# Kernel tuning notes

Hardware: AMD Instinct MI355X
Metric: run time of the kernel (lower is better)

The kernel has to match this reference:

```python
import jax, jax.numpy as jnp
import numpy as np

B, S, H = 512, 50, 20
N_NODE, N_CAT = 100000, 1298
MEM, CLUS = 20, 10
STEP, KBLOCKS = 1, 2
MIX = 0.52  # a = 0.52*attn_last + 0.48*ht


def setup_inputs() -> dict:
    key = jax.random.key(0)
    ks = iter(jax.random.split(key, 48))
    stdv = 1.0 / np.sqrt(H)
    def u(shape):
        return jax.random.uniform(next(ks), shape, jnp.float32, -stdv, stdv)
    inp = {}
    inp['inputs'] = jax.random.randint(next(ks), (B, S), 0, N_NODE, dtype=jnp.int32)
    inp['category'] = jax.random.randint(next(ks), (B, S), 0, N_CAT, dtype=jnp.int32)
    inp['A'] = jax.random.uniform(next(ks), (B, S, 2 * S), jnp.float32)
    inp['mask'] = jnp.ones((B, S), jnp.int32)
    # embeddings
    inp['emb'] = u((N_NODE, H)); inp['emb1'] = u((N_CAT, H))
    # GNN params
    inp['w_ih'] = u((3 * H, 2 * H)); inp['w_hh'] = u((3 * H, H))
    inp['b_ih'] = u((3 * H,)); inp['b_hh'] = u((3 * H,))
    inp['b_iah'] = u((H,)); inp['b_oah'] = u((H,))
    inp['w_ein'] = u((H, H)); inp['b_ein'] = u((H,))
    inp['w_eout'] = u((H, H)); inp['b_eout'] = u((H,))
    # two single-head MHAs
    for p in ('mha', 'mha1'):
        inp[p + '_in_w'] = u((3 * H, H)); inp[p + '_in_b'] = u((3 * H,))
        inp[p + '_out_w'] = u((H, H)); inp[p + '_out_b'] = u((H,))
    # residual blocks
    for p in ('rn', 'rn1'):
        inp[p + '_w1'] = u((H, H)); inp[p + '_b1'] = u((H,))
        inp[p + '_w2'] = u((H, H)); inp[p + '_b2'] = u((H,))
    # memory readout
    inp['mem_M'] = u((CLUS, MEM)); inp['mem_Wa'] = u((2 * H, MEM)); inp['mem_fc'] = u((MEM, MEM))
    # heads
    inp['wc'] = u((H, 3 * H)); inp['bc'] = u((H,))
    inp['wp'] = u((H, 3 * H)); inp['bp'] = u((H,))
    return inp


def _mha(x, w_in, b_in, w_out, b_out):
    # Faithful to torch nn.MultiheadAttention (seq-first, 1 head):
    # x is [B,S,H] but torch treats dim0 as sequence -> attention mixes along axis 0.
    E = x.shape[-1]
    q, k, v = jnp.split(x @ w_in.T + b_in, 3, axis=-1)
    q = q * (1.0 / jnp.sqrt(jnp.float32(E)))
    scores = jnp.einsum('lne,mne->nlm', q, k)        # [S_axis1, L, L]
    attn = jax.nn.softmax(scores, axis=-1)
    out = jnp.einsum('nlm,mne->lne', attn, v)
    return out @ w_out.T + b_out


def _residual(x, w1, b1, w2, b2):
    # eval mode: dropout = identity
    return x + jax.nn.relu(x @ w1.T + b1) @ w2.T + b2


def _gnn_cell(A, h, w_ein, b_ein, w_eout, b_eout, b_iah, b_oah, w_ih, b_ih, w_hh, b_hh):
    s = h.shape[1]
    inp_in = jnp.einsum('bij,bjh->bih', A[:, :, :s], h @ w_ein.T + b_ein) + b_iah
    inp_out = jnp.einsum('bij,bjh->bih', A[:, :, s:2 * s], h @ w_eout.T + b_eout) + b_oah
    gi = jnp.concatenate([inp_in, inp_out], -1) @ w_ih.T + b_ih
    gh = h @ w_hh.T + b_hh
    i_r, i_i, i_n = jnp.split(gi, 3, -1)
    h_r, h_i, h_n = jnp.split(gh, 3, -1)
    r = jax.nn.sigmoid(i_r + h_r)
    z = jax.nn.sigmoid(i_i + h_i)
    n = jnp.tanh(i_n + r * h_n)
    return n + z * (h - n)


def reference(inputs, category, A, mask, emb, emb1, w_ih, w_hh, b_ih, b_hh, b_iah, b_oah,
              w_ein, b_ein, w_eout, b_eout,
              mha_in_w, mha_in_b, mha_out_w, mha_out_b,
              mha1_in_w, mha1_in_b, mha1_out_w, mha1_out_b,
              rn_w1, rn_b1, rn_w2, rn_b2, rn1_w1, rn1_b1, rn1_w2, rn1_b2,
              mem_M, mem_Wa, mem_fc, wc, bc, wp, bp):
    item_h = emb[inputs]          # [B,S,H]
    cat_h = emb1[category]        # [B,S,H]
    for _ in range(STEP):
        item_h = _gnn_cell(A, item_h, w_ein, b_ein, w_eout, b_eout,
                           b_iah, b_oah, w_ih, b_ih, w_hh, b_hh)
    bidx = jnp.arange(mask.shape[0])
    last = jnp.sum(mask, 1) - 1
    ht_item = item_h[bidx, last]
    ht_cat = cat_h[bidx, last]
    x = item_h
    for _ in range(KBLOCKS):
        x = _residual(_mha(x, mha_in_w, mha_in_b, mha_out_w, mha_out_b), rn_w1, rn_b1, rn_w2, rn_b2)
    a_item = MIX * x[bidx, last] + (1 - MIX) * ht_item
    y = cat_h
    for _ in range(KBLOCKS):
        y = _residual(_mha(y, mha1_in_w, mha1_in_b, mha1_out_w, mha1_out_b), rn1_w1, rn1_b1, rn1_w2, rn1_b2)
    a_cat = MIX * y[bidx, last] + (1 - MIX) * ht_cat
    a = jnp.concatenate([a_item, a_cat], -1)                # [B, 2H]
    att = jax.nn.softmax((a @ mem_Wa) @ mem_M.T, axis=-1)   # [B, CLUS]
    reps = jnp.tanh((att @ mem_M) @ mem_fc)                 # [B, MEM]
    car = jnp.concatenate([a, reps], -1)                    # [B, 3H]
    final = jax.nn.sigmoid(car @ wc.T + bc) * (car @ wp.T + bp)
    scores = final @ emb[1:].T                              # [B, N_NODE-1]
    return scores
```

## Files before the change

### kernel.cpp

```cpp
#include <hip/hip_runtime.h>
#include <hip/hip_bf16.h>

#define BB 512
#define SS 50
#define HH 20
#define NN 100000
#define NMC 8
#define MCH 64
#define NRC 4
#define MT 16
#define PBSTRIDE ((size_t)BB*24)

__device__ __forceinline__ float frcp(float x){
#if __has_builtin(__builtin_amdgcn_rcpf)
  return __builtin_amdgcn_rcpf(x);
#else
  return 1.f/x;
#endif
}
__device__ __forceinline__ float fsig(float x){ return frcp(1.f + __expf(-x)); }
__device__ __forceinline__ float ftanh(float x){ return 1.f - 2.f*frcp(1.f + __expf(2.f*x)); }

__global__ __launch_bounds__(256)
void k_gnnqkv(const int* __restrict__ inputs, const int* __restrict__ category,
              const float* __restrict__ A, const int* __restrict__ mask,
              const float* __restrict__ emb, const float* __restrict__ emb1,
              const float* __restrict__ w_ih, const float* __restrict__ w_hh,
              const float* __restrict__ b_ih, const float* __restrict__ b_hh,
              const float* __restrict__ b_iah, const float* __restrict__ b_oah,
              const float* __restrict__ w_ein, const float* __restrict__ b_ein,
              const float* __restrict__ w_eout, const float* __restrict__ b_eout,
              const float* __restrict__ inw0, const float* __restrict__ inb0,
              const float* __restrict__ inw1, const float* __restrict__ inb1,
              float* __restrict__ q_t, float* __restrict__ k_t, float* __restrict__ v_t,
              int* __restrict__ last, float* __restrict__ ht_item, float* __restrict__ ht_cat)
{
    __shared__ float sA[SS*2*SS];
    __shared__ float sit[SS*HH], sct[SS*HH], shin[SS*HH], shout[SS*HH];
    __shared__ float sinp[SS*HH], soutp[SS*HH];
    __shared__ float swein[HH*HH], sweout[HH*HH];
    __shared__ float swih[60*40], swhh[60*HH];
    __shared__ float sw0[60*HH], sw1w[60*HH];
    __shared__ float sbein[HH], sbeout[HH], sbih[60], sbhh[60], sbiah[HH], sboah[HH], sb0[60], sb1b[60];
    __shared__ int slast;
    const int b = blockIdx.x, t = threadIdx.x;

    for (int i=t;i<SS*2*SS;i+=256) sA[i] = A[(size_t)b*SS*2*SS + i];
    for (int i=t;i<HH*HH;i+=256) { swein[i]=w_ein[i]; sweout[i]=w_eout[i]; }
    for (int i=t;i<60*40;i+=256) swih[i]=w_ih[i];
    for (int i=t;i<60*HH;i+=256) { swhh[i]=w_hh[i]; sw0[i]=inw0[i]; sw1w[i]=inw1[i]; }
    if (t<60){ sbih[t]=b_ih[t]; sbhh[t]=b_hh[t]; sb0[t]=inb0[t]; sb1b[t]=inb1[t]; }
    if (t<HH){ sbein[t]=b_ein[t]; sbeout[t]=b_eout[t]; sbiah[t]=b_iah[t]; sboah[t]=b_oah[t]; }
    for (int i=t;i<SS*HH;i+=256){
        int r=i/HH, e=i%HH;
        sit[i]=emb [(size_t)inputs  [b*SS+r]*HH+e];
        sct[i]=emb1[(size_t)category[b*SS+r]*HH+e];
    }
    if (t==0){ int s=0; for (int j=0;j<SS;j++) s+=mask[b*SS+j]; slast=s-1; }
    __syncthreads();

    for (int i=t;i<SS*HH;i+=256){
        int r=i/HH, c=i%HH;
        float si=sbein[c], so=sbeout[c];
        #pragma unroll
        for (int e=0;e<HH;e++){ float hv=sit[r*HH+e]; si+=swein[c*HH+e]*hv; so+=sweout[c*HH+e]*hv; }
        shin[i]=si; shout[i]=so;
    }
    __syncthreads();
    for (int i=t;i<SS*HH;i+=256){
        int r=i/HH, e=i%HH;
        float ai=sbiah[e], ao=sboah[e];
        #pragma unroll 5
        for (int j=0;j<SS;j++){
            ai+=sA[r*2*SS+j]   *shin [j*HH+e];
            ao+=sA[r*2*SS+SS+j]*shout[j*HH+e];
        }
        sinp[i]=ai; soutp[i]=ao;
    }
    __syncthreads();
    float nh[4];
    #pragma unroll
    for (int ii=0;ii<4;ii++){
        int i=t+ii*256;
        if (i<SS*HH){
            int r=i/HH, e=i%HH;
            float gir=sbih[e], gii=sbih[20+e], gin=sbih[40+e];
            #pragma unroll
            for (int k=0;k<HH;k++){
                float vi=sinp[r*HH+k], vo=soutp[r*HH+k];
                gir+=swih[e*40+k]*vi      + swih[e*40+HH+k]*vo;
                gii+=swih[(20+e)*40+k]*vi + swih[(20+e)*40+HH+k]*vo;
                gin+=swih[(40+e)*40+k]*vi + swih[(40+e)*40+HH+k]*vo;
            }
            float ghr=sbhh[e], ghi=sbhh[20+e], ghn=sbhh[40+e];
            #pragma unroll
            for (int k=0;k<HH;k++){
                float hv=sit[r*HH+k];
                ghr+=swhh[e*HH+k]*hv; ghi+=swhh[(20+e)*HH+k]*hv; ghn+=swhh[(40+e)*HH+k]*hv;
            }
            float rr=fsig(gir+ghr), zz=fsig(gii+ghi);
            float nn2=ftanh(gin+rr*ghn);
            nh[ii]=nn2+zz*(sit[i]-nn2);
        }
    }
    __syncthreads();
    #pragma unroll
    for (int ii=0;ii<4;ii++){ int i=t+ii*256; if (i<SS*HH) sit[i]=nh[ii]; }
    __syncthreads();

    if (t<HH)                    ht_item[b*HH+t]      = sit[slast*HH+t];
    else if (t>=32 && t<32+HH)   ht_cat [b*HH+(t-32)] = sct[slast*HH+(t-32)];
    else if (t==63)              last[b]=slast;

    const float SCALE = 0.22360679774997896f;
    for (int oi=t; oi<2*SS*60; oi+=256){
        int p=oi/(SS*60); int rem=oi%(SS*60); int r=rem/60; int c=rem%60;
        const float* src = p? sct  : sit;
        const float* w   = p? sw1w : sw0;
        const float* bb_ = p? sb1b : sb0;
        float acc=bb_[c];
        #pragma unroll
        for (int e=0;e<HH;e++) acc += w[c*HH+e]*src[r*HH+e];
        int which=c/HH, cc=c%HH;
        size_t off=((size_t)(p*SS+r)*BB + b)*HH + cc;
        if (which==0)      q_t[off]=acc*SCALE;
        else if (which==1) k_t[off]=acc;
        else               v_t[off]=acc;
    }
}

__global__ __launch_bounds__(256)
void k_flags(const int* __restrict__ last, int* __restrict__ needed)
{
    __shared__ int nf[SS];
    int t=threadIdx.x;
    if (t<SS) nf[t]=0;
    __syncthreads();
    for (int b=t;b<BB;b+=256){ int l=last[b]; atomicOr(&nf[l],1); }
    __syncthreads();
    if (t<SS) needed[t]=nf[t];
}

__global__ __launch_bounds__(128)
void k_attn(const float* __restrict__ q_t, const float* __restrict__ k_t,
            const float* __restrict__ v_t, const int* __restrict__ needed,
            float* __restrict__ pbuf)
{
    const int s=blockIdx.x, p=blockIdx.y, z=blockIdx.z;
    if (!needed[s]) return;
    const int mc=z>>2, rc=z&3, t=threadIdx.x;
    __shared__ float sk[MCH*HH], sv[MCH*HH];
    const size_t base=(size_t)(p*SS+s)*BB;
    {
        const float4* kb=(const float4*)(k_t+(base+(size_t)mc*MCH)*HH);
        const float4* vb=(const float4*)(v_t+(base+(size_t)mc*MCH)*HH);
        float4* sk4=(float4*)sk; float4* sv4=(float4*)sv;
        for (int i=t;i<MCH*HH/4;i+=128){ sk4[i]=kb[i]; sv4[i]=vb[i]; }
    }
    __syncthreads();
    const int row = rc*128 + t;
    float4 q[5];
    {
        const float4* qp=(const float4*)(q_t+(base+row)*HH);
        #pragma unroll
        for (int i=0;i<5;i++) q[i]=qp[i];
    }
    float4 o[5];
    #pragma unroll
    for (int i=0;i<5;i++) o[i]=make_float4(0.f,0.f,0.f,0.f);
    float mx=-1e30f, sm=0.f;

    for (int mt0=0; mt0<MCH; mt0+=MT){
        float sc[MT]; float tm=-1e30f;
        #pragma unroll
        for (int j=0;j<MT;j++){
            const float4* kr=(const float4*)(sk+(mt0+j)*HH);
            float a0=0.f;
            #pragma unroll
            for (int i=0;i<5;i++){
                float4 kv=kr[i];
                a0+=q[i].x*kv.x+q[i].y*kv.y+q[i].z*kv.z+q[i].w*kv.w;
            }
            sc[j]=a0; tm=fmaxf(tm,a0);
        }
        float nm=fmaxf(mx,tm);
        float c=__expf(mx-nm);
        sm*=c;
        #pragma unroll
        for (int i=0;i<5;i++){ o[i].x*=c; o[i].y*=c; o[i].z*=c; o[i].w*=c; }
        mx=nm;
        #pragma unroll
        for (int j=0;j<MT;j++){
            float pe=__expf(sc[j]-nm);
            sm+=pe;
            const float4* vr=(const float4*)(sv+(mt0+j)*HH);
            #pragma unroll
            for (int i=0;i<5;i++){
                float4 vv=vr[i];
                o[i].x+=pe*vv.x; o[i].y+=pe*vv.y; o[i].z+=pe*vv.z; o[i].w+=pe*vv.w;
            }
        }
    }
    float* pb = pbuf + (((size_t)(p*SS+s)*NMC+mc)*BB + row)*24;
    float4* w0=(float4*)pb;
    w0[0]=make_float4(mx,sm,o[0].x,o[0].y);
    w0[1]=make_float4(o[0].z,o[0].w,o[1].x,o[1].y);
    w0[2]=make_float4(o[1].z,o[1].w,o[2].x,o[2].y);
    w0[3]=make_float4(o[2].z,o[2].w,o[3].x,o[3].y);
    w0[4]=make_float4(o[3].z,o[3].w,o[4].x,o[4].y);
    w0[5]=make_float4(o[4].z,o[4].w,0.f,0.f);
}

__device__ __forceinline__ void merge_res(const float* __restrict__ pbase,
    const float* __restrict__ sow, const float* __restrict__ sob,
    const float* __restrict__ sw1, const float* __restrict__ sb1,
    const float* __restrict__ sw2, const float* __restrict__ sb2,
    float* __restrict__ xo)
{
    float mx=-1e30f;
    #pragma unroll
    for (int mc2=0;mc2<NMC;mc2++) mx=fmaxf(mx, pbase[mc2*PBSTRIDE]);
    float sum=0.f, o[HH];
    #pragma unroll
    for (int e=0;e<HH;e++) o[e]=0.f;
    #pragma unroll
    for (int mc2=0;mc2<NMC;mc2++){
        const float4* pc=(const float4*)(pbase+mc2*PBSTRIDE);
        float4 a=pc[0], b4=pc[1], c4=pc[2], d4=pc[3], e4=pc[4], f4=pc[5];
        float cc=__expf(a.x-mx);
        sum+=a.y*cc;
        o[0]+=a.z*cc;  o[1]+=a.w*cc;
        o[2]+=b4.x*cc; o[3]+=b4.y*cc; o[4]+=b4.z*cc; o[5]+=b4.w*cc;
        o[6]+=c4.x*cc; o[7]+=c4.y*cc; o[8]+=c4.z*cc; o[9]+=c4.w*cc;
        o[10]+=d4.x*cc; o[11]+=d4.y*cc; o[12]+=d4.z*cc; o[13]+=d4.w*cc;
        o[14]+=e4.x*cc; o[15]+=e4.y*cc; o[16]+=e4.z*cc; o[17]+=e4.w*cc;
        o[18]+=f4.x*cc; o[19]+=f4.y*cc;
    }
    float inv=frcp(sum);
    float ao[HH];
    #pragma unroll
    for (int e=0;e<HH;e++) ao[e]=o[e]*inv;
    float mo[HH];
    #pragma unroll
    for (int e=0;e<HH;e++){
        float acc=sob[e];
        #pragma unroll
        for (int f=0;f<HH;f++) acc+=sow[e*HH+f]*ao[f];
        mo[e]=acc;
    }
    float u[HH];
    #pragma unroll
    for (int g=0;g<HH;g++){
        float acc=sb1[g];
        #pragma unroll
        for (int f=0;f<HH;f++) acc+=sw1[g*HH+f]*mo[f];
        u[g]=fmaxf(acc,0.f);
    }
    #pragma unroll
    for (int e=0;e<HH;e++){
        float acc=mo[e]+sb2[e];
        #pragma unroll
        for (int g=0;g<HH;g++) acc+=sw2[e*HH+g]*u[g];
        xo[e]=acc;
    }
}

__global__ __launch_bounds__(256)
void k_finqkv(const float* __restrict__ pbuf, const int* __restrict__ needed,
    const float* __restrict__ ow0, const float* __restrict__ ob0,
    const float* __restrict__ w10, const float* __restrict__ b10,
    const float* __restrict__ w20, const float* __restrict__ b20,
    const float* __restrict__ iw0, const float* __restrict__ ib0,
    const float* __restrict__ ow1, const float* __restrict__ ob1,
    const float* __restrict__ w11, const float* __restrict__ b11,
    const float* __restrict__ w21, const float* __restrict__ b21,
    const float* __restrict__ iw1, const float* __restrict__ ib1,
    float* __restrict__ q_t, float* __restrict__ k_t, float* __restrict__ v_t)
{
    const int s=blockIdx.x>>1;
    if (!needed[s]) return;
    __shared__ float sow[400], sw1[400], sw2[400], siw[1200];
    __shared__ float sob[20], sb1[20], sb2[20], sib[60];
    const int p=blockIdx.y, t=threadIdx.x;
    const int b=(blockIdx.x&1)*256+t;
    const float* OW=p?ow1:ow0; const float* OB=p?ob1:ob0;
    const float* W1=p?w11:w10; const float* B1=p?b11:b10;
    const float* W2=p?w21:w20; const float* B2=p?b21:b20;
    const float* IW=p?iw1:iw0; const float* IB=p?ib1:ib0;
    for (int i=t;i<400;i+=256){ sow[i]=OW[i]; sw1[i]=W1[i]; sw2[i]=W2[i]; }
    for (int i=t;i<1200;i+=256) siw[i]=IW[i];
    if (t<20){ sob[t]=OB[t]; sb1[t]=B1[t]; sb2[t]=B2[t]; }
    if (t<60) sib[t]=IB[t];
    __syncthreads();
    const float* pbase = pbuf + (((size_t)(p*SS+s)*NMC)*BB + b)*24;
    float xo[HH];
    merge_res(pbase, sow,sob,sw1,sb1,sw2,sb2, xo);
    const float SCALE = 0.22360679774997896f;
    size_t off0=((size_t)(p*SS+s)*BB + b)*HH;
    #pragma unroll
    for (int c=0;c<HH;c++){
        float aq=sib[c], ak=sib[20+c], av=sib[40+c];
        #pragma unroll
        for (int e=0;e<HH;e++){ float xv=xo[e]; aq+=siw[c*HH+e]*xv; ak+=siw[(20+c)*HH+e]*xv; av+=siw[(40+c)*HH+e]*xv; }
        q_t[off0+c]=aq*SCALE; k_t[off0+c]=ak; v_t[off0+c]=av;
    }
}

__global__ __launch_bounds__(256)
void k_fin(const float* __restrict__ pbuf, const int* __restrict__ needed,
    const int* __restrict__ last,
    const float* __restrict__ ht_item, const float* __restrict__ ht_cat,
    const float* __restrict__ ow0, const float* __restrict__ ob0,
    const float* __restrict__ w10, const float* __restrict__ b10,
    const float* __restrict__ w20, const float* __restrict__ b20,
    const float* __restrict__ ow1, const float* __restrict__ ob1,
    const float* __restrict__ w11, const float* __restrict__ b11,
    const float* __restrict__ w21, const float* __restrict__ b21,
    float* __restrict__ a_out)
{
    const int s=blockIdx.x>>1;
    if (!needed[s]) return;
    __shared__ float sow[400], sw1[400], sw2[400];
    __shared__ float sob[20], sb1[20], sb2[20];
    const int p=blockIdx.y, t=threadIdx.x;
    const int b=(blockIdx.x&1)*256+t;
    const float* OW=p?ow1:ow0; const float* OB=p?ob1:ob0;
    const float* W1=p?w11:w10; const float* B1=p?b11:b10;
    const float* W2=p?w21:w20; const float* B2=p?b21:b20;
    for (int i=t;i<400;i+=256){ sow[i]=OW[i]; sw1[i]=W1[i]; sw2[i]=W2[i]; }
    if (t<20){ sob[t]=OB[t]; sb1[t]=B1[t]; sb2[t]=B2[t]; }
    __syncthreads();
    if (last[b] != s) return;
    const float* pbase = pbuf + (((size_t)(p*SS+s)*NMC)*BB + b)*24;
    float xo[HH];
    merge_res(pbase, sow,sob,sw1,sb1,sw2,sb2, xo);
    const float* ht = p? ht_cat : ht_item;
    #pragma unroll
    for (int e=0;e<HH;e++)
        a_out[(size_t)b*40 + p*HH + e] = 0.52f*xo[e] + 0.48f*ht[b*HH+e];
}

__global__ __launch_bounds__(64)
void k_head(const float* __restrict__ a_in,
            const float* __restrict__ mem_M, const float* __restrict__ mem_Wa,
            const float* __restrict__ mem_fc,
            const float* __restrict__ wc, const float* __restrict__ bc,
            const float* __restrict__ wp, const float* __restrict__ bp,
            float* __restrict__ final_)
{
    int b=blockIdx.x*64+threadIdx.x;
    if (b>=BB) return;
    float a[40];
    const float4* a4=(const float4*)(a_in+(size_t)b*40);
    #pragma unroll
    for (int i=0;i<10;i++){ float4 v=a4[i]; a[4*i]=v.x; a[4*i+1]=v.y; a[4*i+2]=v.z; a[4*i+3]=v.w; }
    float t20[20];
    #pragma unroll
    for (int j=0;j<20;j++){
        float acc=0.f;
        #pragma unroll
        for (int k=0;k<40;k++) acc+=a[k]*mem_Wa[k*20+j];
        t20[j]=acc;
    }
    float lg[10]; float mxv=-1e30f;
    #pragma unroll
    for (int c=0;c<10;c++){
        float acc=0.f;
        #pragma unroll
        for (int j=0;j<20;j++) acc+=t20[j]*mem_M[c*20+j];
        lg[c]=acc; mxv=fmaxf(mxv,acc);
    }
    float se=0.f;
    #pragma unroll
    for (int c=0;c<10;c++){ lg[c]=__expf(lg[c]-mxv); se+=lg[c]; }
    float inv=frcp(se);
    #pragma unroll
    for (int c=0;c<10;c++) lg[c]*=inv;
    float am[20];
    #pragma unroll
    for (int j=0;j<20;j++){
        float acc=0.f;
        #pragma unroll
        for (int c=0;c<10;c++) acc+=lg[c]*mem_M[c*20+j];
        am[j]=acc;
    }
    float reps[20];
    #pragma unroll
    for (int j2=0;j2<20;j2++){
        float acc=0.f;
        #pragma unroll
        for (int j=0;j<20;j++) acc+=am[j]*mem_fc[j*20+j2];
        reps[j2]=ftanh(acc);
    }
    #pragma unroll
    for (int e=0;e<HH;e++){
        float c1=bc[e], c2=bp[e];
        #pragma unroll
        for (int k=0;k<40;k++){ c1+=a[k]*wc[e*60+k]; c2+=a[k]*wp[e*60+k]; }
        #pragma unroll
        for (int k=0;k<20;k++){ c1+=reps[k]*wc[e*60+40+k]; c2+=reps[k]*wp[e*60+40+k]; }
        final_[b*HH+e]=fsig(c1)*c2;
    }
}

__global__ __launch_bounds__(256)
void k_scores(const float* __restrict__ final_, const float* __restrict__ emb,
              float* __restrict__ out)
{
    int node = blockIdx.x*256 + threadIdx.x;
    if (node >= NN-1) return;
    float4 er[5];
    const float4* e4 = (const float4*)(emb + ((size_t)node + 1)*HH);
    #pragma unroll
    for (int i=0;i<5;i++) er[i]=e4[i];
    float* op = out + node;
    for (int b = 0; b < BB; b++) {
        const float4* fb = (const float4*)(final_ + b*HH);
        float acc = 0.f;
        #pragma unroll
        for (int i=0;i<5;i++){
            float4 f=fb[i];
            acc += f.x*er[i].x + f.y*er[i].y + f.z*er[i].z + f.w*er[i].w;
        }
        *op = acc;
        op += (NN-1);
    }
}

extern "C" void kernel_launch(void* const* d_in, const int* in_sizes, int n_in,
                              void* d_out, int out_size, void* d_ws, size_t ws_size,
                              hipStream_t stream) {
    const int*   inputs   = (const int*)  d_in[0];
    const int*   category = (const int*)  d_in[1];
    const float* A        = (const float*)d_in[2];
    const int*   mask     = (const int*)  d_in[3];
    const float* emb      = (const float*)d_in[4];
    const float* emb1     = (const float*)d_in[5];
    const float* w_ih     = (const float*)d_in[6];
    const float* w_hh     = (const float*)d_in[7];
    const float* b_ih     = (const float*)d_in[8];
    const float* b_hh     = (const float*)d_in[9];
    const float* b_iah    = (const float*)d_in[10];
    const float* b_oah    = (const float*)d_in[11];
    const float* w_ein    = (const float*)d_in[12];
    const float* b_ein    = (const float*)d_in[13];
    const float* w_eout   = (const float*)d_in[14];
    const float* b_eout   = (const float*)d_in[15];
    const float* mha_in_w  = (const float*)d_in[16];
    const float* mha_in_b  = (const float*)d_in[17];
    const float* mha_out_w = (const float*)d_in[18];
    const float* mha_out_b = (const float*)d_in[19];
    const float* mha1_in_w  = (const float*)d_in[20];
    const float* mha1_in_b  = (const float*)d_in[21];
    const float* mha1_out_w = (const float*)d_in[22];
    const float* mha1_out_b = (const float*)d_in[23];
    const float* rn_w1 = (const float*)d_in[24];
    const float* rn_b1 = (const float*)d_in[25];
    const float* rn_w2 = (const float*)d_in[26];
    const float* rn_b2 = (const float*)d_in[27];
    const float* rn1_w1 = (const float*)d_in[28];
    const float* rn1_b1 = (const float*)d_in[29];
    const float* rn1_w2 = (const float*)d_in[30];
    const float* rn1_b2 = (const float*)d_in[31];
    const float* mem_M  = (const float*)d_in[32];
    const float* mem_Wa = (const float*)d_in[33];
    const float* mem_fc = (const float*)d_in[34];
    const float* wc = (const float*)d_in[35];
    const float* bc = (const float*)d_in[36];
    const float* wp = (const float*)d_in[37];
    const float* bp = (const float*)d_in[38];
    float* out = (float*)d_out;

    float* W = (float*)d_ws;
    float* q_t     = W;
    float* k_t     = W + 1024000;
    float* v_t     = W + 2048000;
    float* pbuf    = W + 3072000;
    float* ht_item = W + 12902400;
    float* ht_cat  = W + 12912640;
    float* a_buf   = W + 12922880;
    float* final_  = W + 12943360;
    int*   last    = (int*)(W + 12953600);
    int*   needed  = (int*)(W + 12954112);

    k_gnnqkv<<<BB, 256, 0, stream>>>(inputs, category, A, mask, emb, emb1,
                                     w_ih, w_hh, b_ih, b_hh, b_iah, b_oah,
                                     w_ein, b_ein, w_eout, b_eout,
                                     mha_in_w, mha_in_b, mha1_in_w, mha1_in_b,
                                     q_t, k_t, v_t, last, ht_item, ht_cat);
    k_flags<<<1, 256, 0, stream>>>(last, needed);
    k_attn<<<dim3(SS,2,NMC*NRC), 128, 0, stream>>>(q_t, k_t, v_t, needed, pbuf);
    k_finqkv<<<dim3(100,2), 256, 0, stream>>>(pbuf, needed,
        mha_out_w, mha_out_b, rn_w1, rn_b1, rn_w2, rn_b2, mha_in_w, mha_in_b,
        mha1_out_w, mha1_out_b, rn1_w1, rn1_b1, rn1_w2, rn1_b2, mha1_in_w, mha1_in_b,
        q_t, k_t, v_t);
    k_attn<<<dim3(SS,2,NMC*NRC), 128, 0, stream>>>(q_t, k_t, v_t, needed, pbuf);
    k_fin<<<dim3(100,2), 256, 0, stream>>>(pbuf, needed, last, ht_item, ht_cat,
        mha_out_w, mha_out_b, rn_w1, rn_b1, rn_w2, rn_b2,
        mha1_out_w, mha1_out_b, rn1_w1, rn1_b1, rn1_w2, rn1_b2,
        a_buf);
    k_head<<<8, 64, 0, stream>>>(a_buf, mem_M, mem_Wa, mem_fc, wc, bc, wp, bp, final_);
    k_scores<<<(NN-1+255)/256, 256, 0, stream>>>(final_, emb, out);
}
```

Before: 582.7 us.

## Fuse attention, merge and head stages into persistent kernel with grid barriers

```diff
diff --git a/kernel.cpp b/kernel.cpp
--- a/kernel.cpp
+++ b/kernel.cpp
@@ -7,8 +7,8 @@
 #define NN 100000
 #define NMC 8
 #define MCH 64
-#define NRC 4
 #define MT 16
+#define NB_MEGA 128
 #define PBSTRIDE ((size_t)BB*24)
 
 __device__ __forceinline__ float frcp(float x){
@@ -33,7 +33,8 @@
               const float* __restrict__ inw0, const float* __restrict__ inb0,
               const float* __restrict__ inw1, const float* __restrict__ inb1,
               float* __restrict__ q_t, float* __restrict__ k_t, float* __restrict__ v_t,
-              int* __restrict__ last, float* __restrict__ ht_item, float* __restrict__ ht_cat)
+              int* __restrict__ last, float* __restrict__ ht_item, float* __restrict__ ht_cat,
+              int* __restrict__ bar)
 {
     __shared__ float sA[SS*2*SS];
     __shared__ float sit[SS*HH], sct[SS*HH], shin[SS*HH], shout[SS*HH];
@@ -45,6 +46,8 @@
     __shared__ int slast;
     const int b = blockIdx.x, t = threadIdx.x;
 
+    if (b==0 && t<8) bar[t] = 0;
+
     for (int i=t;i<SS*2*SS;i+=256) sA[i] = A[(size_t)b*SS*2*SS + i];
     for (int i=t;i<HH*HH;i+=256) { swein[i]=w_ein[i]; sweout[i]=w_eout[i]; }
     for (int i=t;i<60*40;i+=256) swih[i]=w_ih[i];
@@ -129,86 +132,16 @@
     }
 }
 
-__global__ __launch_bounds__(256)
-void k_flags(const int* __restrict__ last, int* __restrict__ needed)
-{
-    __shared__ int nf[SS];
-    int t=threadIdx.x;
-    if (t<SS) nf[t]=0;
-    __syncthreads();
-    for (int b=t;b<BB;b+=256){ int l=last[b]; atomicOr(&nf[l],1); }
-    __syncthreads();
-    if (t<SS) needed[t]=nf[t];
-}
-
-__global__ __launch_bounds__(128)
-void k_attn(const float* __restrict__ q_t, const float* __restrict__ k_t,
-            const float* __restrict__ v_t, const int* __restrict__ needed,
-            float* __restrict__ pbuf)
-{
-    const int s=blockIdx.x, p=blockIdx.y, z=blockIdx.z;
-    if (!needed[s]) return;
-    const int mc=z>>2, rc=z&3, t=threadIdx.x;
-    __shared__ float sk[MCH*HH], sv[MCH*HH];
-    const size_t base=(size_t)(p*SS+s)*BB;
-    {
-        const float4* kb=(const float4*)(k_t+(base+(size_t)mc*MCH)*HH);
-        const float4* vb=(const float4*)(v_t+(base+(size_t)mc*MCH)*HH);
-        float4* sk4=(float4*)sk; float4* sv4=(float4*)sv;
-        for (int i=t;i<MCH*HH/4;i+=128){ sk4[i]=kb[i]; sv4[i]=vb[i]; }
-    }
-    __syncthreads();
-    const int row = rc*128 + t;
-    float4 q[5];
-    {
-        const float4* qp=(const float4*)(q_t+(base+row)*HH);
-        #pragma unroll
-        for (int i=0;i<5;i++) q[i]=qp[i];
-    }
-    float4 o[5];
-    #pragma unroll
-    for (int i=0;i<5;i++) o[i]=make_float4(0.f,0.f,0.f,0.f);
-    float mx=-1e30f, sm=0.f;
-
-    for (int mt0=0; mt0<MCH; mt0+=MT){
-        float sc[MT]; float tm=-1e30f;
-        #pragma unroll
-        for (int j=0;j<MT;j++){
-            const float4* kr=(const float4*)(sk+(mt0+j)*HH);
-            float a0=0.f;
-            #pragma unroll
-            for (int i=0;i<5;i++){
-                float4 kv=kr[i];
-                a0+=q[i].x*kv.x+q[i].y*kv.y+q[i].z*kv.z+q[i].w*kv.w;
-            }
-            sc[j]=a0; tm=fmaxf(tm,a0);
-        }
-        float nm=fmaxf(mx,tm);
-        float c=__expf(mx-nm);
-        sm*=c;
-        #pragma unroll
-        for (int i=0;i<5;i++){ o[i].x*=c; o[i].y*=c; o[i].z*=c; o[i].w*=c; }
-        mx=nm;
-        #pragma unroll
-        for (int j=0;j<MT;j++){
-            float pe=__expf(sc[j]-nm);
-            sm+=pe;
-            const float4* vr=(const float4*)(sv+(mt0+j)*HH);
-            #pragma unroll
-            for (int i=0;i<5;i++){
-                float4 vv=vr[i];
-                o[i].x+=pe*vv.x; o[i].y+=pe*vv.y; o[i].z+=pe*vv.z; o[i].w+=pe*vv.w;
-            }
-        }
-    }
-    float* pb = pbuf + (((size_t)(p*SS+s)*NMC+mc)*BB + row)*24;
-    float4* w0=(float4*)pb;
-    w0[0]=make_float4(mx,sm,o[0].x,o[0].y);
-    w0[1]=make_float4(o[0].z,o[0].w,o[1].x,o[1].y);
-    w0[2]=make_float4(o[1].z,o[1].w,o[2].x,o[2].y);
-    w0[3]=make_float4(o[2].z,o[2].w,o[3].x,o[3].y);
-    w0[4]=make_float4(o[3].z,o[3].w,o[4].x,o[4].y);
-    w0[5]=make_float4(o[4].z,o[4].w,0.f,0.f);
+__device__ __forceinline__ void gridbar(int* bar, int idx){
+    __syncthreads();
+    if (threadIdx.x==0){
+        __threadfence();
+        __hip_atomic_fetch_add(&bar[idx], 1, __ATOMIC_RELEASE, __HIP_MEMORY_SCOPE_AGENT);
+        while (__hip_atomic_load(&bar[idx], __ATOMIC_ACQUIRE, __HIP_MEMORY_SCOPE_AGENT) < NB_MEGA)
+            __builtin_amdgcn_s_sleep(2);
+        __threadfence();
+    }
+    __syncthreads();
 }
 
 __device__ __forceinline__ void merge_res(const float* __restrict__ pbase,
@@ -265,141 +198,247 @@
     }
 }
 
+__device__ __forceinline__ void attn_task(const float* __restrict__ q_t,
+    const float* __restrict__ k_t, const float* __restrict__ v_t,
+    float* __restrict__ pbuf, float* __restrict__ sk, float* __restrict__ sv,
+    int si, int p, int rc, int mc, int t)
+{
+    const size_t base=(size_t)(p*SS+si)*BB;
+    {
+        const float4* kb=(const float4*)(k_t+(base+(size_t)mc*MCH)*HH);
+        const float4* vb=(const float4*)(v_t+(base+(size_t)mc*MCH)*HH);
+        float4* sk4=(float4*)sk; float4* sv4=(float4*)sv;
+        for (int i=t;i<MCH*HH/4;i+=256){ sk4[i]=kb[i]; sv4[i]=vb[i]; }
+    }
+    __syncthreads();
+    const int row = rc*256 + t;
+    float4 q[5];
+    {
+        const float4* qp=(const float4*)(q_t+(base+row)*HH);
+        #pragma unroll
+        for (int i=0;i<5;i++) q[i]=qp[i];
+    }
+    float4 o[5];
+    #pragma unroll
+    for (int i=0;i<5;i++) o[i]=make_float4(0.f,0.f,0.f,0.f);
+    float mx=-1e30f, sm=0.f;
+
+    for (int mt0=0; mt0<MCH; mt0+=MT){
+        float sc[MT]; float tm=-1e30f;
+        #pragma unroll
+        for (int j=0;j<MT;j++){
+            const float4* kr=(const float4*)(sk+(mt0+j)*HH);
+            float a0=0.f;
+            #pragma unroll
+            for (int i=0;i<5;i++){
+                float4 kv=kr[i];
+                a0+=q[i].x*kv.x+q[i].y*kv.y+q[i].z*kv.z+q[i].w*kv.w;
+            }
+            sc[j]=a0; tm=fmaxf(tm,a0);
+        }
+        float nm=fmaxf(mx,tm);
+        float c=__expf(mx-nm);
+        sm*=c;
+        #pragma unroll
+        for (int i=0;i<5;i++){ o[i].x*=c; o[i].y*=c; o[i].z*=c; o[i].w*=c; }
+        mx=nm;
+        #pragma unroll
+        for (int j=0;j<MT;j++){
+            float pe=__expf(sc[j]-nm);
+            sm+=pe;
+            const float4* vr=(const float4*)(sv+(mt0+j)*HH);
+            #pragma unroll
+            for (int i=0;i<5;i++){
+                float4 vv=vr[i];
+                o[i].x+=pe*vv.x; o[i].y+=pe*vv.y; o[i].z+=pe*vv.z; o[i].w+=pe*vv.w;
+            }
+        }
+    }
+    float* pb = pbuf + (((size_t)(p*SS+si)*NMC+mc)*BB + row)*24;
+    float4* w0=(float4*)pb;
+    w0[0]=make_float4(mx,sm,o[0].x,o[0].y);
+    w0[1]=make_float4(o[0].z,o[0].w,o[1].x,o[1].y);
+    w0[2]=make_float4(o[1].z,o[1].w,o[2].x,o[2].y);
+    w0[3]=make_float4(o[2].z,o[2].w,o[3].x,o[3].y);
+    w0[4]=make_float4(o[3].z,o[3].w,o[4].x,o[4].y);
+    w0[5]=make_float4(o[4].z,o[4].w,0.f,0.f);
+    __syncthreads();
+}
+
 __global__ __launch_bounds__(256)
-void k_finqkv(const float* __restrict__ pbuf, const int* __restrict__ needed,
-    const float* __restrict__ ow0, const float* __restrict__ ob0,
-    const float* __restrict__ w10, const float* __restrict__ b10,
-    const float* __restrict__ w20, const float* __restrict__ b20,
-    const float* __restrict__ iw0, const float* __restrict__ ib0,
-    const float* __restrict__ ow1, const float* __restrict__ ob1,
-    const float* __restrict__ w11, const float* __restrict__ b11,
-    const float* __restrict__ w21, const float* __restrict__ b21,
-    const float* __restrict__ iw1, const float* __restrict__ ib1,
-    float* __restrict__ q_t, float* __restrict__ k_t, float* __restrict__ v_t)
-{
-    const int s=blockIdx.x>>1;
-    if (!needed[s]) return;
-    __shared__ float sow[400], sw1[400], sw2[400], siw[1200];
-    __shared__ float sob[20], sb1[20], sb2[20], sib[60];
-    const int p=blockIdx.y, t=threadIdx.x;
-    const int b=(blockIdx.x&1)*256+t;
-    const float* OW=p?ow1:ow0; const float* OB=p?ob1:ob0;
-    const float* W1=p?w11:w10; const float* B1=p?b11:b10;
-    const float* W2=p?w21:w20; const float* B2=p?b21:b20;
-    const float* IW=p?iw1:iw0; const float* IB=p?ib1:ib0;
-    for (int i=t;i<400;i+=256){ sow[i]=OW[i]; sw1[i]=W1[i]; sw2[i]=W2[i]; }
-    for (int i=t;i<1200;i+=256) siw[i]=IW[i];
-    if (t<20){ sob[t]=OB[t]; sb1[t]=B1[t]; sb2[t]=B2[t]; }
-    if (t<60) sib[t]=IB[t];
-    __syncthreads();
-    const float* pbase = pbuf + (((size_t)(p*SS+s)*NMC)*BB + b)*24;
-    float xo[HH];
-    merge_res(pbase, sow,sob,sw1,sb1,sw2,sb2, xo);
-    const float SCALE = 0.22360679774997896f;
-    size_t off0=((size_t)(p*SS+s)*BB + b)*HH;
-    #pragma unroll
-    for (int c=0;c<HH;c++){
-        float aq=sib[c], ak=sib[20+c], av=sib[40+c];
-        #pragma unroll
-        for (int e=0;e<HH;e++){ float xv=xo[e]; aq+=siw[c*HH+e]*xv; ak+=siw[(20+c)*HH+e]*xv; av+=siw[(40+c)*HH+e]*xv; }
-        q_t[off0+c]=aq*SCALE; k_t[off0+c]=ak; v_t[off0+c]=av;
-    }
-}
-
-__global__ __launch_bounds__(256)
-void k_fin(const float* __restrict__ pbuf, const int* __restrict__ needed,
-    const int* __restrict__ last,
-    const float* __restrict__ ht_item, const float* __restrict__ ht_cat,
-    const float* __restrict__ ow0, const float* __restrict__ ob0,
-    const float* __restrict__ w10, const float* __restrict__ b10,
-    const float* __restrict__ w20, const float* __restrict__ b20,
-    const float* __restrict__ ow1, const float* __restrict__ ob1,
-    const float* __restrict__ w11, const float* __restrict__ b11,
-    const float* __restrict__ w21, const float* __restrict__ b21,
-    float* __restrict__ a_out)
-{
-    const int s=blockIdx.x>>1;
-    if (!needed[s]) return;
-    __shared__ float sow[400], sw1[400], sw2[400];
-    __shared__ float sob[20], sb1[20], sb2[20];
-    const int p=blockIdx.y, t=threadIdx.x;
-    const int b=(blockIdx.x&1)*256+t;
-    const float* OW=p?ow1:ow0; const float* OB=p?ob1:ob0;
-    const float* W1=p?w11:w10; const float* B1=p?b11:b10;
-    const float* W2=p?w21:w20; const float* B2=p?b21:b20;
-    for (int i=t;i<400;i+=256){ sow[i]=OW[i]; sw1[i]=W1[i]; sw2[i]=W2[i]; }
-    if (t<20){ sob[t]=OB[t]; sb1[t]=B1[t]; sb2[t]=B2[t]; }
-    __syncthreads();
-    if (last[b] != s) return;
-    const float* pbase = pbuf + (((size_t)(p*SS+s)*NMC)*BB + b)*24;
-    float xo[HH];
-    merge_res(pbase, sow,sob,sw1,sb1,sw2,sb2, xo);
-    const float* ht = p? ht_cat : ht_item;
-    #pragma unroll
-    for (int e=0;e<HH;e++)
-        a_out[(size_t)b*40 + p*HH + e] = 0.52f*xo[e] + 0.48f*ht[b*HH+e];
-}
-
-__global__ __launch_bounds__(64)
-void k_head(const float* __restrict__ a_in,
+void k_mega(const float* __restrict__ q_t0, float* __restrict__ q_t,
+            float* __restrict__ k_t, float* __restrict__ v_t,
+            float* __restrict__ pbuf, const int* __restrict__ last,
+            const float* __restrict__ ht_item, const float* __restrict__ ht_cat,
+            const float* __restrict__ ow0, const float* __restrict__ ob0,
+            const float* __restrict__ w10, const float* __restrict__ b10,
+            const float* __restrict__ w20, const float* __restrict__ b20,
+            const float* __restrict__ iw0, const float* __restrict__ ib0,
+            const float* __restrict__ ow1, const float* __restrict__ ob1,
+            const float* __restrict__ w11, const float* __restrict__ b11,
+            const float* __restrict__ w21, const float* __restrict__ b21,
+            const float* __restrict__ iw1, const float* __restrict__ ib1,
             const float* __restrict__ mem_M, const float* __restrict__ mem_Wa,
             const float* __restrict__ mem_fc,
             const float* __restrict__ wc, const float* __restrict__ bc,
             const float* __restrict__ wp, const float* __restrict__ bp,
-            float* __restrict__ final_)
+            float* __restrict__ final_, int* __restrict__ bar)
 {
-    int b=blockIdx.x*64+threadIdx.x;
-    if (b>=BB) return;
-    float a[40];
-    const float4* a4=(const float4*)(a_in+(size_t)b*40);
-    #pragma unroll
-    for (int i=0;i<10;i++){ float4 v=a4[i]; a[4*i]=v.x; a[4*i+1]=v.y; a[4*i+2]=v.z; a[4*i+3]=v.w; }
-    float t20[20];
-    #pragma unroll
-    for (int j=0;j<20;j++){
-        float acc=0.f;
-        #pragma unroll
-        for (int k=0;k<40;k++) acc+=a[k]*mem_Wa[k*20+j];
-        t20[j]=acc;
-    }
-    float lg[10]; float mxv=-1e30f;
-    #pragma unroll
-    for (int c=0;c<10;c++){
-        float acc=0.f;
-        #pragma unroll
-        for (int j=0;j<20;j++) acc+=t20[j]*mem_M[c*20+j];
-        lg[c]=acc; mxv=fmaxf(mxv,acc);
-    }
-    float se=0.f;
-    #pragma unroll
-    for (int c=0;c<10;c++){ lg[c]=__expf(lg[c]-mxv); se+=lg[c]; }
-    float inv=frcp(se);
-    #pragma unroll
-    for (int c=0;c<10;c++) lg[c]*=inv;
-    float am[20];
-    #pragma unroll
-    for (int j=0;j<20;j++){
-        float acc=0.f;
-        #pragma unroll
-        for (int c=0;c<10;c++) acc+=lg[c]*mem_M[c*20+j];
-        am[j]=acc;
-    }
-    float reps[20];
-    #pragma unroll
-    for (int j2=0;j2<20;j2++){
-        float acc=0.f;
-        #pragma unroll
-        for (int j=0;j<20;j++) acc+=am[j]*mem_fc[j*20+j2];
-        reps[j2]=ftanh(acc);
-    }
-    #pragma unroll
-    for (int e=0;e<HH;e++){
-        float c1=bc[e], c2=bp[e];
-        #pragma unroll
-        for (int k=0;k<40;k++){ c1+=a[k]*wc[e*60+k]; c2+=a[k]*wp[e*60+k]; }
-        #pragma unroll
-        for (int k=0;k<20;k++){ c1+=reps[k]*wc[e*60+40+k]; c2+=reps[k]*wp[e*60+40+k]; }
-        final_[b*HH+e]=fsig(c1)*c2;
+    __shared__ float smem[6400];
+    __shared__ int slast_c[BB];
+    __shared__ int snf[SS];
+    __shared__ int slist[SS];
+    __shared__ int sns;
+    const int t = threadIdx.x, bid = blockIdx.x;
+
+    for (int i=t;i<BB;i+=256) slast_c[i]=last[i];
+    if (t<SS) snf[t]=0;
+    __syncthreads();
+    for (int i=t;i<BB;i+=256) atomicOr(&snf[slast_c[i]],1);
+    __syncthreads();
+    if (t==0){ int c=0; for (int s=0;s<SS;s++) if (snf[s]) slist[c++]=s; sns=c; }
+    __syncthreads();
+    const int ns = sns;
+
+    {
+        const int T = ns*2*16;
+        float* sk = smem; float* sv = smem + MCH*HH;
+        for (int task=bid; task<T; task+=NB_MEGA){
+            int si=slist[task/32]; int rem=task%32;
+            int p=rem>>4, rc=(rem>>3)&1, mc=rem&7;
+            attn_task(q_t0, k_t, v_t, pbuf, sk, sv, si, p, rc, mc, t);
+        }
+    }
+    gridbar(bar, 0);
+
+    {
+        const int T = ns*2*2;
+        float* sow=smem; float* sw1=smem+400; float* sw2=smem+800; float* siw=smem+1200;
+        float* sob=smem+2400; float* sb1=smem+2420; float* sb2=smem+2440; float* sib=smem+2460;
+        for (int task=bid; task<T; task+=NB_MEGA){
+            int si=slist[task/4]; int p=(task>>1)&1; int bc=task&1;
+            const float* OW=p?ow1:ow0; const float* OB=p?ob1:ob0;
+            const float* W1=p?w11:w10; const float* B1=p?b11:b10;
+            const float* W2=p?w21:w20; const float* B2=p?b21:b20;
+            const float* IW=p?iw1:iw0; const float* IB=p?ib1:ib0;
+            __syncthreads();
+            for (int i=t;i<400;i+=256){ sow[i]=OW[i]; sw1[i]=W1[i]; sw2[i]=W2[i]; }
+            for (int i=t;i<1200;i+=256) siw[i]=IW[i];
+            if (t<20){ sob[t]=OB[t]; sb1[t]=B1[t]; sb2[t]=B2[t]; }
+            if (t<60) sib[t]=IB[t];
+            __syncthreads();
+            const int b = bc*256 + t;
+            const float* pbase = pbuf + (((size_t)(p*SS+si)*NMC)*BB + b)*24;
+            float xo[HH];
+            merge_res(pbase, sow,sob,sw1,sb1,sw2,sb2, xo);
+            const float SCALE = 0.22360679774997896f;
+            size_t off0=((size_t)(p*SS+si)*BB + b)*HH;
+            #pragma unroll
+            for (int c=0;c<HH;c++){
+                float aq=sib[c], ak=sib[20+c], av=sib[40+c];
+                #pragma unroll
+                for (int e=0;e<HH;e++){ float xv=xo[e]; aq+=siw[c*HH+e]*xv; ak+=siw[(20+c)*HH+e]*xv; av+=siw[(40+c)*HH+e]*xv; }
+                q_t[off0+c]=aq*SCALE; k_t[off0+c]=ak; v_t[off0+c]=av;
+            }
+        }
+    }
+    gridbar(bar, 1);
+
+    {
+        const int T = ns*2*16;
+        float* sk = smem; float* sv = smem + MCH*HH;
+        for (int task=bid; task<T; task+=NB_MEGA){
+            int si=slist[task/32]; int rem=task%32;
+            int p=rem>>4, rc=(rem>>3)&1, mc=rem&7;
+            attn_task(q_t, k_t, v_t, pbuf, sk, sv, si, p, rc, mc, t);
+        }
+    }
+    gridbar(bar, 2);
+
+    {
+        for (int task=bid; task<2; task+=NB_MEGA){
+            __syncthreads();
+            for (int i=t;i<200;i+=256)  smem[i]     =mem_M[i];
+            for (int i=t;i<800;i+=256)  smem[200+i] =mem_Wa[i];
+            for (int i=t;i<400;i+=256)  smem[1000+i]=mem_fc[i];
+            for (int i=t;i<1200;i+=256){ smem[1400+i]=wc[i]; smem[2600+i]=wp[i]; }
+            if (t<20){ smem[3800+t]=bc[t]; smem[3820+t]=bp[t]; }
+            for (int i=t;i<400;i+=256){
+                smem[3840+i]=ow0[i]; smem[3840+400+i]=w10[i]; smem[3840+800+i]=w20[i];
+                smem[5100+i]=ow1[i]; smem[5100+400+i]=w11[i]; smem[5100+800+i]=w21[i];
+            }
+            if (t<20){
+                smem[3840+1200+t]=ob0[t]; smem[3840+1220+t]=b10[t]; smem[3840+1240+t]=b20[t];
+                smem[5100+1200+t]=ob1[t]; smem[5100+1220+t]=b11[t]; smem[5100+1240+t]=b21[t];
+            }
+            __syncthreads();
+            const int b = task*256 + t;
+            const int sb = slast_c[b];
+            float a[40];
+            {
+                const float* pb0 = pbuf + (((size_t)(0*SS+sb)*NMC)*BB + b)*24;
+                float xo[HH];
+                merge_res(pb0, smem+3840, smem+3840+1200, smem+3840+400, smem+3840+1220,
+                          smem+3840+800, smem+3840+1240, xo);
+                #pragma unroll
+                for (int e=0;e<HH;e++) a[e] = 0.52f*xo[e] + 0.48f*ht_item[b*HH+e];
+            }
+            {
+                const float* pb1 = pbuf + (((size_t)(1*SS+sb)*NMC)*BB + b)*24;
+                float xo[HH];
+                merge_res(pb1, smem+5100, smem+5100+1200, smem+5100+400, smem+5100+1220,
+                          smem+5100+800, smem+5100+1240, xo);
+                #pragma unroll
+                for (int e=0;e<HH;e++) a[20+e] = 0.52f*xo[e] + 0.48f*ht_cat[b*HH+e];
+            }
+            float t20[20];
+            #pragma unroll
+            for (int j=0;j<20;j++){
+                float acc=0.f;
+                #pragma unroll
+                for (int k=0;k<40;k++) acc+=a[k]*smem[200+k*20+j];
+                t20[j]=acc;
+            }
+            float lg[10]; float mxv=-1e30f;
+            #pragma unroll
+            for (int c=0;c<10;c++){
+                float acc=0.f;
+                #pragma unroll
+                for (int j=0;j<20;j++) acc+=t20[j]*smem[c*20+j];
+                lg[c]=acc; mxv=fmaxf(mxv,acc);
+            }
+            float se=0.f;
+            #pragma unroll
+            for (int c=0;c<10;c++){ lg[c]=__expf(lg[c]-mxv); se+=lg[c]; }
+            float inv=frcp(se);
+            #pragma unroll
+            for (int c=0;c<10;c++) lg[c]*=inv;
+            float am[20];
+            #pragma unroll
+            for (int j=0;j<20;j++){
+                float acc=0.f;
+                #pragma unroll
+                for (int c=0;c<10;c++) acc+=lg[c]*smem[c*20+j];
+                am[j]=acc;
+            }
+            float reps[20];
+            #pragma unroll
+            for (int j2=0;j2<20;j2++){
+                float acc=0.f;
+                #pragma unroll
+                for (int j=0;j<20;j++) acc+=am[j]*smem[1000+j*20+j2];
+                reps[j2]=ftanh(acc);
+            }
+            #pragma unroll
+            for (int e=0;e<HH;e++){
+                float c1=smem[3800+e], c2=smem[3820+e];
+                #pragma unroll
+                for (int k=0;k<40;k++){ c1+=a[k]*smem[1400+e*60+k]; c2+=a[k]*smem[2600+e*60+k]; }
+                #pragma unroll
+                for (int k=0;k<20;k++){ c1+=reps[k]*smem[1400+e*60+40+k]; c2+=reps[k]*smem[2600+e*60+40+k]; }
+                final_[b*HH+e]=fsig(c1)*c2;
+            }
+        }
     }
 }
 
@@ -478,27 +517,19 @@
     float* pbuf    = W + 3072000;
     float* ht_item = W + 12902400;
     float* ht_cat  = W + 12912640;
-    float* a_buf   = W + 12922880;
-    float* final_  = W + 12943360;
-    int*   last    = (int*)(W + 12953600);
-    int*   needed  = (int*)(W + 12954112);
+    float* final_  = W + 12922880;
+    int*   last    = (int*)(W + 12933120);
+    int*   bar     = (int*)(W + 12933632);
 
     k_gnnqkv<<<BB, 256, 0, stream>>>(inputs, category, A, mask, emb, emb1,
                                      w_ih, w_hh, b_ih, b_hh, b_iah, b_oah,
                                      w_ein, b_ein, w_eout, b_eout,
                                      mha_in_w, mha_in_b, mha1_in_w, mha1_in_b,
-                                     q_t, k_t, v_t, last, ht_item, ht_cat);
-    k_flags<<<1, 256, 0, stream>>>(last, needed);
-    k_attn<<<dim3(SS,2,NMC*NRC), 128, 0, stream>>>(q_t, k_t, v_t, needed, pbuf);
-    k_finqkv<<<dim3(100,2), 256, 0, stream>>>(pbuf, needed,
+                                     q_t, k_t, v_t, last, ht_item, ht_cat, bar);
+    k_mega<<<NB_MEGA, 256, 0, stream>>>(q_t, q_t, k_t, v_t, pbuf, last,
+        ht_item, ht_cat,
         mha_out_w, mha_out_b, rn_w1, rn_b1, rn_w2, rn_b2, mha_in_w, mha_in_b,
         mha1_out_w, mha1_out_b, rn1_w1, rn1_b1, rn1_w2, rn1_b2, mha1_in_w, mha1_in_b,
-        q_t, k_t, v_t);
-    k_attn<<<dim3(SS,2,NMC*NRC), 128, 0, stream>>>(q_t, k_t, v_t, needed, pbuf);
-    k_fin<<<dim3(100,2), 256, 0, stream>>>(pbuf, needed, last, ht_item, ht_cat,
-        mha_out_w, mha_out_b, rn_w1, rn_b1, rn_w2, rn_b2,
-        mha1_out_w, mha1_out_b, rn1_w1, rn1_b1, rn1_w2, rn1_b2,
-        a_buf);
-    k_head<<<8, 64, 0, stream>>>(a_buf, mem_M, mem_Wa, mem_fc, wc, bc, wp, bp, final_);
+        mem_M, mem_Wa, mem_fc, wc, bc, wp, bp, final_, bar);
     k_scores<<<(NN-1+255)/256, 256, 0, stream>>>(final_, emb, out);
 }
```

New measurement: 605.0 us. 3.8% more time.
